# Kernel optimization log

Measured on AMD Instinct MI355X. Metric: run time of the kernel, lower is better.

Reference implementation:

```python
import jax, jax.numpy as jnp
import numpy as np

B, S, D, H, E, K = 2, 2048, 1024, 8, 4, 2
DH = D // H  # 128


def setup_inputs() -> dict:
    key = jax.random.key(0)
    ks = jax.random.split(key, 9)
    std = 1.0 / np.sqrt(D)
    return {
        "q_src": jax.random.normal(ks[0], (B, S, D), jnp.float32),
        "k_src": jax.random.normal(ks[1], (B, S, D), jnp.float32),
        "v_src": jax.random.normal(ks[2], (B, S, D), jnp.float32),
        "Wq": jax.random.normal(ks[3], (H * DH, D), jnp.float32) * std,
        "Wk": jax.random.normal(ks[4], (H * DH, D), jnp.float32) * std,
        "Wv": jax.random.normal(ks[5], (H, E, D, DH), jnp.float32) * std,   # per-head, per-expert V proj
        "Wo": jax.random.normal(ks[6], (H, E, DH, D), jnp.float32) * (1.0 / np.sqrt(H * DH)),
        "sel_v": jax.random.normal(ks[7], (H * E, D), jnp.float32) * std,   # V-expert router
        "sel_o": jax.random.normal(ks[8], (H * E, D), jnp.float32) * std,   # O-expert router
    }


def reference(q_src, k_src, v_src, Wq, Wk, Wv, Wo, sel_v, sel_o):
    s = DH ** -0.25  # scale.sqrt() applied to both q and k -> combined 1/sqrt(d_head)

    q = (q_src @ Wq.T * s).reshape(B, S, H, DH).transpose(0, 2, 1, 3)  # [B,H,S,DH]
    k = (k_src @ Wk.T * s).reshape(B, S, H, DH).transpose(0, 2, 1, 3)

    # --- V expert routing: sigmoid gate + top-k over experts, per head ---
    gv_all = jax.nn.sigmoid((k_src @ sel_v.T).reshape(B, S, H, E))
    gv, iv = jax.lax.top_k(gv_all, K)                                  # [B,S,H,K]
    # per-expert V projection (equiv. to CVMM grouped-GEMM), then gather selected experts
    v_all = jnp.einsum('bsd,hedk->bshek', v_src, Wv)                   # [B,S,H,E,DH]
    v = (jnp.take_along_axis(v_all, iv[..., None], axis=3) * gv[..., None]).sum(3)
    v = v.transpose(0, 2, 1, 3)                                        # [B,H,S,DH]

    # --- attention (mask=None; base class attend() is abstract, plain SDPA) ---
    scores = jnp.einsum('bhqd,bhkd->bhqk', q, k)
    att = jax.nn.softmax(scores, axis=-1)
    res = jnp.einsum('bhqk,bhkd->bhqd', att, v).transpose(0, 2, 1, 3)  # [B,S,H,DH]

    # --- O expert routing: weighted sum over heads and selected output experts ---
    go_all = jax.nn.sigmoid((q_src @ sel_o.T).reshape(B, S, H, E))
    go, io = jax.lax.top_k(go_all, K)                                  # [B,S,H,K]
    gd = (go[..., None] * jax.nn.one_hot(io, E, dtype=res.dtype)).sum(-2)  # dense gates [B,S,H,E]
    gated = res[:, :, :, None, :] * gd[..., None]                      # [B,S,H,E,DH]
    out = jnp.einsum('bshed,hedo->bso', gated, Wo)                     # [B,S,D]
    return out
```

## Files before the change

kernel.cpp:

```cpp
#include <hip/hip_runtime.h>

#define BB 2
#define SS 2048
#define DD 1024
#define HH 8
#define EE 4
#define DHH 128
#define RR (BB*SS)

typedef __attribute__((ext_vector_type(8))) short short8;
typedef __attribute__((ext_vector_type(4))) short short4v;
typedef __attribute__((ext_vector_type(4))) float f32x4;

__device__ __forceinline__ float b2f(short x) {
    unsigned u = ((unsigned)(unsigned short)x) << 16;
    return __uint_as_float(u);
}
__device__ __forceinline__ short f2bf(float f) {
    unsigned u = __float_as_uint(f);
    unsigned r = (u + 0x7fffu + ((u >> 16) & 1u)) >> 16;
    return (short)(unsigned short)r;
}

__device__ __forceinline__ void gl_lds16(const short* g, short* l) {
    __builtin_amdgcn_global_load_lds(
        (const __attribute__((address_space(1))) unsigned int*)g,
        (__attribute__((address_space(3))) unsigned int*)l,
        16, 0, 0);
}

template <bool BF16_OUT>
__device__ __forceinline__ void gemm16_body(
    short* As, short* Bs,
    const short* __restrict__ A, const short* __restrict__ Bm, void* __restrict__ Cv,
    int Kd, int lda, int ldb, int ldc, float alpha, int bm0, int bn0)
{
    const int t = threadIdx.x;
    const int lane = t & 63, wave = t >> 6;
    const int lm = lane & 15, quad = lane >> 4;
    const int wm = (wave >> 1) * 64, wn = (wave & 1) * 64;
    f32x4 acc[4][4] = {};

    const int srow = t >> 2, scol = (t & 3) * 8;
    const short* Ag = A + (long)(bm0 + srow) * lda + scol;
    const short* Bg = Bm + (long)(bn0 + srow) * ldb + scol;
    const long ldaH = (long)lda * 64, ldbH = (long)ldb * 64;
    short* Asd = As + srow * 32 + scol;
    short* Bsd = Bs + srow * 32 + scol;

    for (int k0 = 0; k0 < Kd; k0 += 32) {
        __syncthreads();
        gl_lds16(Ag + k0,        Asd);
        gl_lds16(Ag + k0 + ldaH, Asd + 64 * 32);
        gl_lds16(Bg + k0,        Bsd);
        gl_lds16(Bg + k0 + ldbH, Bsd + 64 * 32);
        __syncthreads();

        short8 af[4], bf[4];
#pragma unroll
        for (int i = 0; i < 4; i++)
            af[i] = *(const short8*)&As[(wm + i * 16 + lm) * 32 + quad * 8];
#pragma unroll
        for (int j = 0; j < 4; j++)
            bf[j] = *(const short8*)&Bs[(wn + j * 16 + lm) * 32 + quad * 8];
#pragma unroll
        for (int i = 0; i < 4; i++)
#pragma unroll
            for (int j = 0; j < 4; j++)
                acc[i][j] = __builtin_amdgcn_mfma_f32_16x16x32_bf16(
                    af[i], bf[j], acc[i][j], 0, 0, 0);
    }
#pragma unroll
    for (int i = 0; i < 4; i++) {
#pragma unroll
        for (int j = 0; j < 4; j++) {
            int n = bn0 + wn + j * 16 + lm;
#pragma unroll
            for (int r = 0; r < 4; r++) {
                int m = bm0 + wm + i * 16 + quad * 4 + r;
                float v = acc[i][j][r] * alpha;
                if (BF16_OUT) ((short*)Cv)[(long)m * ldc + n] = f2bf(v);
                else          ((float*)Cv)[(long)m * ldc + n] = v;
            }
        }
    }
}

__global__ __launch_bounds__(256)
void shc_gemm_bt16(const short* __restrict__ A, const short* __restrict__ Bm,
                   void* __restrict__ Cv, int Kd, int lda, int ldb, int ldc,
                   float alpha)
{
    __shared__ short As[128 * 32];
    __shared__ short Bs[128 * 32];
    gemm16_body<true>(As, Bs, A, Bm, Cv, Kd, lda, ldb, ldc, alpha,
                      blockIdx.y * 128, blockIdx.x * 128);
}

__global__ __launch_bounds__(256)
void shc_gemm_qk(const short* __restrict__ Qs, const short* __restrict__ Ks,
                 const short* __restrict__ Wq16, const short* __restrict__ Wk16,
                 short* __restrict__ Qo, short* __restrict__ Ko, float alpha)
{
    __shared__ short As[128 * 32];
    __shared__ short Bs[128 * 32];
    if (blockIdx.z == 0)
        gemm16_body<true>(As, Bs, Qs, Wq16, Qo, 1024, 1024, 1024, 1024,
                          alpha, blockIdx.y * 128, blockIdx.x * 128);
    else
        gemm16_body<true>(As, Bs, Ks, Wk16, Ko, 1024, 1024, 1024, 1024,
                          alpha, blockIdx.y * 128, blockIdx.x * 128);
}

__global__ __launch_bounds__(256)
void shc_gemm_out(const short* __restrict__ X, const short* __restrict__ WoT,
                  float* __restrict__ out, float* __restrict__ P1)
{
    __shared__ short As[128 * 32];
    __shared__ short Bs[128 * 32];
    const int koff = blockIdx.z * 2048;
    float* C = blockIdx.z ? P1 : out;
    gemm16_body<false>(As, Bs, X + koff, WoT + koff, C,
                       2048, 4096, 4096, 1024, 1.0f,
                       blockIdx.y * 128, blockIdx.x * 128);
}

__global__ __launch_bounds__(256)
void shc_add(float* __restrict__ out, const float* __restrict__ P1)
{
    long i = ((long)blockIdx.x * 256 + threadIdx.x) * 4;
    f32x4 a = *(const f32x4*)(out + i);
    f32x4 b = *(const f32x4*)(P1 + i);
#pragma unroll
    for (int j = 0; j < 4; j++) a[j] += b[j];
    *(f32x4*)(out + i) = a;
}

__global__ __launch_bounds__(256)
void shc_cvt3(const float* __restrict__ a, const float* __restrict__ b,
              const float* __restrict__ c, short* __restrict__ oa,
              short* __restrict__ ob, short* __restrict__ oc)
{
    const float* src = blockIdx.z == 0 ? a : (blockIdx.z == 1 ? b : c);
    short* dst       = blockIdx.z == 0 ? oa : (blockIdx.z == 1 ? ob : oc);
    long i = ((long)blockIdx.x * 256 + threadIdx.x) * 8;
    f32x4 f0 = *(const f32x4*)(src + i);
    f32x4 f1 = *(const f32x4*)(src + i + 4);
    short8 o;
#pragma unroll
    for (int j = 0; j < 4; j++) {
        o[j]     = f2bf(f0[j]);
        o[4 + j] = f2bf(f1[j]);
    }
    *(short8*)(dst + i) = o;
}

__global__ __launch_bounds__(256)
void shc_gates4(const float* __restrict__ q_src, const float* __restrict__ k_src,
                const float* __restrict__ sel_v, const float* __restrict__ sel_o,
                float* __restrict__ gv_d, float* __restrict__ go_d)
{
    const int t = threadIdx.x, lane = t & 63, wave = t >> 6;
    const int bid = blockIdx.x;
    const int s = bid & 1;
    const int r0 = (bid >> 1) * 8 + wave * 2;
    const float* srcb = s ? q_src : k_src;
    const float* selb = s ? sel_o : sel_v;

    double S0[16], S1[16];
#pragma unroll
    for (int i = 0; i < 4; i++) {
        f32x4 v0 = *(const f32x4*)(srcb + (long)r0 * 1024 + lane * 16 + i * 4);
        f32x4 v1 = *(const f32x4*)(srcb + (long)(r0 + 1) * 1024 + lane * 16 + i * 4);
#pragma unroll
        for (int j = 0; j < 4; j++) {
            S0[i * 4 + j] = (double)v0[j];
            S1[i * 4 + j] = (double)v1[j];
        }
    }

    float myv = 0.f;
#pragma unroll 2
    for (int o = 0; o < 32; ++o) {
        f32x4 W[4];
#pragma unroll
        for (int i = 0; i < 4; i++)
            W[i] = *(const f32x4*)(selb + o * 1024 + lane * 16 + i * 4);
        double a0 = 0.0, a1 = 0.0;
#pragma unroll
        for (int i = 0; i < 4; i++)
#pragma unroll
            for (int j = 0; j < 4; j++) {
                double w = (double)W[i][j];
                a0 += S0[i * 4 + j] * w;
                a1 += S1[i * 4 + j] * w;
            }
        a0 += __shfl_xor(a0, 1);  a1 += __shfl_xor(a1, 1);
        a0 += __shfl_xor(a0, 2);  a1 += __shfl_xor(a1, 2);
        a0 += __shfl_xor(a0, 4);  a1 += __shfl_xor(a1, 4);
        a0 += __shfl_xor(a0, 8);  a1 += __shfl_xor(a1, 8);
        a0 += __shfl_xor(a0, 16); a1 += __shfl_xor(a1, 16);
        double tcross = (lane < 32) ? a1 : a0;
        double u = __shfl_xor(tcross, 32);
        double tot = ((lane < 32) ? a0 : a1) + u;
        myv = ((lane & 31) == o) ? (float)tot : myv;
    }

    float sg = 1.f / (1.f + __expf(-myv));
    float g1 = __shfl_xor(sg, 1);
    float g2 = __shfl_xor(sg, 2);
    float g3 = __shfl_xor(sg, 3);
    const int e = lane & 3;
    int rank = 0;
    rank += (g1 > sg) || (g1 == sg && (e ^ 1) < e);
    rank += (g2 > sg) || (g2 == sg && (e ^ 2) < e);
    rank += (g3 > sg) || (g3 == sg && (e ^ 3) < e);
    const long row = r0 + (lane >> 5);
    float* outp = (s ? go_d : gv_d) + row * 32 + (lane & 31);
    *outp = (rank < 2) ? sg : 0.f;
}

__global__ __launch_bounds__(256)
void shc_transpose_w(const float* __restrict__ Wv, short* __restrict__ WvT,
                     const float* __restrict__ Wo, short* __restrict__ WoT)
{
    __shared__ float Ls[32][33];
    const int t = threadIdx.x;
    const int rr = t >> 3, cc = (t & 7) * 4;
    const int bid = blockIdx.x;
    if (bid < 4096) {
        const int dhT = bid & 3, dT = (bid >> 2) & 31, he = bid >> 7;
        const int d0 = dT * 32, dh0 = dhT * 32;
        f32x4 vin = *(const f32x4*)(Wv + (long)(he * 1024 + d0 + rr) * 128 + dh0 + cc);
#pragma unroll
        for (int j = 0; j < 4; j++) Ls[rr][cc + j] = vin[j];
        __syncthreads();
        short4v ov;
#pragma unroll
        for (int j = 0; j < 4; j++) ov[j] = f2bf(Ls[cc + j][rr]);
        *(short4v*)(WvT + (long)(he * 128 + dh0 + rr) * 1024 + d0 + cc) = ov;
    } else {
        const int b2 = bid - 4096;
        const int oT = b2 & 31, kT = b2 >> 5;
        const int k0 = kT * 32, o0 = oT * 32;
        f32x4 vin = *(const f32x4*)(Wo + (long)(k0 + rr) * 1024 + o0 + cc);
#pragma unroll
        for (int j = 0; j < 4; j++) Ls[rr][cc + j] = vin[j];
        __syncthreads();
        short4v ov;
#pragma unroll
        for (int j = 0; j < 4; j++) ov[j] = f2bf(Ls[cc + j][rr]);
        *(short4v*)(WoT + (long)(o0 + rr) * 4096 + k0 + cc) = ov;
    }
}

__global__ __launch_bounds__(256)
void shc_combine_vt(const short* __restrict__ v_all, const float* __restrict__ gv_d,
                    short* __restrict__ Vt)
{
    __shared__ short Ls[64 * 136];
    const int t = threadIdx.x;
    const int blk = blockIdx.x;
    const int st = blk & 31, h = (blk >> 5) & 7, b = blk >> 8;
    const int s0 = st * 64;
    const int sl = t >> 2, dh0 = (t & 3) * 32;
    const long row = (long)(b * SS) + s0 + sl;
    const float* g = gv_d + row * 32 + h * 4;
    float g0 = g[0], g1 = g[1], g2 = g[2], g3 = g[3];
    const short* va = v_all + row * 4096 + h * 512;
#pragma unroll
    for (int j = 0; j < 4; j++) {
        int dh = dh0 + j * 8;
        short8 e0 = *(const short8*)(va + 0 * 128 + dh);
        short8 e1 = *(const short8*)(va + 1 * 128 + dh);
        short8 e2 = *(const short8*)(va + 2 * 128 + dh);
        short8 e3 = *(const short8*)(va + 3 * 128 + dh);
        short8 outv;
#pragma unroll
        for (int i = 0; i < 8; i++)
            outv[i] = f2bf(g0 * b2f(e0[i]) + g1 * b2f(e1[i])
                         + g2 * b2f(e2[i]) + g3 * b2f(e3[i]));
        *(short8*)&Ls[sl * 136 + dh] = outv;
    }
    __syncthreads();
    const int dh = t >> 1, sc0 = (t & 1) * 32;
    short* op = Vt + ((long)(b * HH + h) * DHH + dh) * SS + s0 + sc0;
#pragma unroll
    for (int j = 0; j < 4; j++) {
        short8 ov;
#pragma unroll
        for (int i = 0; i < 8; i++)
            ov[i] = Ls[(sc0 + j * 8 + i) * 136 + dh];
        *(short8*)(op + j * 8) = ov;
    }
}

__global__ __launch_bounds__(256)
void shc_attn_mfma(const short* __restrict__ Q, const short* __restrict__ Kg,
                   const short* __restrict__ Vt, const float* __restrict__ go_d,
                   short* __restrict__ X)
{
    __shared__ __align__(16) char smem[40960];
    short* Ks = (short*)smem;
    short* Vs = (short*)(smem + 16384);
    const int t = threadIdx.x;
    const int lane = t & 63, wave = t >> 6;
    const int lm = lane & 15, quad = lane >> 4;
    short* Pw = (short*)(smem + 32768) + wave * 16 * 64;
    const int blk = blockIdx.x;
    const int qt = blk & 31, h = (blk >> 5) & 7, b = blk >> 8;
    const int q0 = qt * 64 + wave * 16;
    const short* Qb = Q + ((long)(b * SS) + q0) * DD + h * DHH;
    const short* Kb = Kg + (long)(b * SS) * DD + h * DHH;
    const short* Vb = Vt + (long)(b * HH + h) * DHH * SS;

    short8 af[4];
#pragma unroll
    for (int c = 0; c < 4; c++)
        af[c] = *(const short8*)(Qb + (long)lm * DD + c * 32 + quad * 8);

    f32x4 o_acc[8] = {};
    float l_lane[4] = {0.f, 0.f, 0.f, 0.f};

    const int ksrow = t >> 2, kscol = (t & 3) * 32;
    const int vsrow = t >> 1, vscol = (t & 1) * 32;
    const int kswz = (ksrow & 7) << 3;
    const int vswz = (vsrow & 7) << 3;
    const int lmswz = (lm & 7) << 3;

    short8 kv[4], vv[4];
#pragma unroll
    for (int j = 0; j < 4; j++) {
        kv[j] = *(const short8*)(Kb + (long)ksrow * DD + kscol + j * 8);
        vv[j] = *(const short8*)(Vb + (long)vsrow * SS + vscol + j * 8);
    }

    for (int kt = 0; kt < SS / 64; ++kt) {
        __syncthreads();
#pragma unroll
        for (int j = 0; j < 4; j++) {
            *(short8*)&Ks[ksrow * 128 + ((kscol + j * 8) ^ kswz)] = kv[j];
            *(short8*)&Vs[vsrow * 64  + ((vscol + j * 8) ^ vswz)] = vv[j];
        }
        __syncthreads();

        const int ktn = (kt + 1) & 31;
#pragma unroll
        for (int j = 0; j < 4; j++) {
            kv[j] = *(const short8*)(Kb + (long)(ktn * 64 + ksrow) * DD + kscol + j * 8);
            vv[j] = *(const short8*)(Vb + (long)vsrow * SS + ktn * 64 + vscol + j * 8);
        }

#pragma unroll
        for (int f = 0; f < 4; f++) {
            f32x4 acc = {-10.f, -10.f, -10.f, -10.f};
#pragma unroll
            for (int c = 0; c < 4; c++) {
                short8 bf = *(const short8*)&Ks[(f * 16 + lm) * 128
                                                + ((c * 32 + quad * 8) ^ lmswz)];
                acc = __builtin_amdgcn_mfma_f32_16x16x32_bf16(af[c], bf, acc, 0, 0, 0);
            }
#pragma unroll
            for (int r = 0; r < 4; r++) {
                float p = __expf(acc[r]);
                l_lane[r] += p;
                const int prow = quad * 4 + r;
                Pw[prow * 64 + ((f * 16 + lm) ^ ((prow & 7) << 3))] = f2bf(p);
            }
        }

        short8 ap0 = *(const short8*)&Pw[lm * 64 + ((quad * 8) ^ lmswz)];
        short8 ap1 = *(const short8*)&Pw[lm * 64 + ((32 + quad * 8) ^ lmswz)];
#pragma unroll
        for (int d = 0; d < 8; d++) {
            short8 bv0 = *(const short8*)&Vs[(d * 16 + lm) * 64 + ((quad * 8) ^ lmswz)];
            short8 bv1 = *(const short8*)&Vs[(d * 16 + lm) * 64 + ((32 + quad * 8) ^ lmswz)];
            o_acc[d] = __builtin_amdgcn_mfma_f32_16x16x32_bf16(ap0, bv0, o_acc[d], 0, 0, 0);
            o_acc[d] = __builtin_amdgcn_mfma_f32_16x16x32_bf16(ap1, bv1, o_acc[d], 0, 0, 0);
        }
    }

    float inv_r[4];
#pragma unroll
    for (int r = 0; r < 4; r++) {
        float l = l_lane[r];
        l += __shfl_xor(l, 1);
        l += __shfl_xor(l, 2);
        l += __shfl_xor(l, 4);
        l += __shfl_xor(l, 8);
        inv_r[r] = 1.f / l;
    }

    __syncthreads();
    float* Of = (float*)smem;
#pragma unroll
    for (int r = 0; r < 4; r++) {
#pragma unroll
        for (int d = 0; d < 8; d++)
            Of[(wave * 16 + quad * 4 + r) * 132 + d * 16 + lm] = o_acc[d][r] * inv_r[r];
    }
    __syncthreads();
    const int xr = t >> 2, xc0 = (t & 3) * 8;
    const long grow = (long)(b * SS) + qt * 64 + xr;
    const float* go4 = go_d + grow * 32 + h * 4;
    float gg[4] = {go4[0], go4[1], go4[2], go4[3]};
    short* Xp = X + grow * 4096 + h * 512;
#pragma unroll
    for (int e = 0; e < 4; e++) {
#pragma unroll
        for (int j = 0; j < 4; j++) {
            int c = xc0 + 32 * j;
            f32x4 f0 = *(const f32x4*)&Of[xr * 132 + c];
            f32x4 f1 = *(const f32x4*)&Of[xr * 132 + c + 4];
            short8 s;
#pragma unroll
            for (int i = 0; i < 4; i++) {
                s[i]     = f2bf(f0[i] * gg[e]);
                s[4 + i] = f2bf(f1[i] * gg[e]);
            }
            *(short8*)(Xp + e * 128 + c) = s;
        }
    }
}

extern "C" void kernel_launch(void* const* d_in, const int* in_sizes, int n_in,
                              void* d_out, int out_size, void* d_ws, size_t ws_size,
                              hipStream_t stream)
{
    const float* q_src = (const float*)d_in[0];
    const float* k_src = (const float*)d_in[1];
    const float* v_src = (const float*)d_in[2];
    const float* Wq    = (const float*)d_in[3];
    const float* Wk    = (const float*)d_in[4];
    const float* Wv    = (const float*)d_in[5];
    const float* Wo    = (const float*)d_in[6];
    const float* sel_v = (const float*)d_in[7];
    const float* sel_o = (const float*)d_in[8];
    float* out = (float*)d_out;
    char* ws = (char*)d_ws;

    short* Qb16 = (short*)(ws + 0);
    short* Kb16 = (short*)(ws + 8388608);
    short* Vtg  = (short*)(ws + 16777216);
    short* Vs16 = (short*)(ws + 16777216);
    short* Vall = (short*)(ws + 25165824);
    short* X    = (short*)(ws + 25165824);
    short* Wq16 = (short*)(ws + 25165824);
    short* Wk16 = (short*)(ws + 27262976);
    float* P1   = (float*)(ws + 58720256);
    short* Qs16 = (short*)(ws + 58720256);
    short* Ks16 = (short*)(ws + 67108864);
    short* WvT  = (short*)(ws + 75497472);
    short* WoT  = (short*)(ws + 83886080);
    float* GVd  = (float*)(ws + 92274688);
    float* GOd  = (float*)(ws + 92798976);

    const float s_scale = 0.29730177875068026f;

    dim3 blk(256);
    shc_cvt3<<<dim3(2048, 1, 3), blk, 0, stream>>>(q_src, k_src, v_src, Qs16, Ks16, Vs16);
    shc_cvt3<<<dim3(512, 1, 2), blk, 0, stream>>>(Wq, Wk, Wk, Wq16, Wk16, Wk16);
    shc_gemm_qk<<<dim3(8, 32, 2), blk, 0, stream>>>(Qs16, Ks16, Wq16, Wk16, Qb16, Kb16, s_scale);
    shc_gates4<<<1024, blk, 0, stream>>>(q_src, k_src, sel_v, sel_o, GVd, GOd);
    shc_transpose_w<<<8192, blk, 0, stream>>>(Wv, WvT, Wo, WoT);
    shc_gemm_bt16<<<dim3(32, 32), blk, 0, stream>>>(Vs16, WvT, Vall, 1024, 1024, 1024, 4096, 1.0f);
    shc_combine_vt<<<512, blk, 0, stream>>>(Vall, GVd, Vtg);
    shc_attn_mfma<<<512, blk, 0, stream>>>(Qb16, Kb16, Vtg, GOd, X);
    shc_gemm_out<<<dim3(8, 32, 2), blk, 0, stream>>>(X, WoT, out, P1);
    shc_add<<<4096, blk, 0, stream>>>(out, P1);
}
```

Measured before the change: 410.3 us.

## Process 32 query rows per wave, load K/V tiles via direct LDS loads, fold log2e

The attention kernel now handles 128 query rows per block (32 per wave as two 16-row MFMA sub-blocks), so each K/V tile staged in LDS is reused by twice as many queries and the grid is halved to 256 blocks. The register-staged K/V prefetch is replaced by direct global-to-LDS loads (gl_lds16) with XOR swizzled addressing, which drops the software double-buffer. The log2(e) factor is folded into the Q/K scale so the kernel can use exp2f instead of __expf. In exchange there is higher register pressure (launch_bounds 256,1), less latency hiding because global loads are no longer overlapped with compute, and only 256 blocks to spread across the device.

Measured after the change: 426.4 us. +3.9%, slower.

```diff
diff --git a/kernel.cpp b/kernel.cpp
--- a/kernel.cpp
+++ b/kernel.cpp
@@ -295,130 +295,142 @@
     }
 }
 
-__global__ __launch_bounds__(256)
+#define NEG10L2E -14.426950408889634f
+__global__ __launch_bounds__(256, 1)
 void shc_attn_mfma(const short* __restrict__ Q, const short* __restrict__ Kg,
                    const short* __restrict__ Vt, const float* __restrict__ go_d,
                    short* __restrict__ X)
 {
-    __shared__ __align__(16) char smem[40960];
+    __shared__ __align__(16) char smem[49152];
     short* Ks = (short*)smem;
     short* Vs = (short*)(smem + 16384);
     const int t = threadIdx.x;
     const int lane = t & 63, wave = t >> 6;
     const int lm = lane & 15, quad = lane >> 4;
-    short* Pw = (short*)(smem + 32768) + wave * 16 * 64;
+    short* Pw = (short*)(smem + 32768) + wave * 2048;
     const int blk = blockIdx.x;
-    const int qt = blk & 31, h = (blk >> 5) & 7, b = blk >> 8;
-    const int q0 = qt * 64 + wave * 16;
+    const int qt = blk & 15, h = (blk >> 4) & 7, b = blk >> 7;
+    const int q0 = qt * 128 + wave * 32;
     const short* Qb = Q + ((long)(b * SS) + q0) * DD + h * DHH;
     const short* Kb = Kg + (long)(b * SS) * DD + h * DHH;
     const short* Vb = Vt + (long)(b * HH + h) * DHH * SS;
 
-    short8 af[4];
-#pragma unroll
-    for (int c = 0; c < 4; c++)
-        af[c] = *(const short8*)(Qb + (long)lm * DD + c * 32 + quad * 8);
-
-    f32x4 o_acc[8] = {};
-    float l_lane[4] = {0.f, 0.f, 0.f, 0.f};
-
-    const int ksrow = t >> 2, kscol = (t & 3) * 32;
-    const int vsrow = t >> 1, vscol = (t & 1) * 32;
-    const int kswz = (ksrow & 7) << 3;
-    const int vswz = (vsrow & 7) << 3;
+    short8 af[2][4];
+#pragma unroll
+    for (int qb = 0; qb < 2; qb++)
+#pragma unroll
+        for (int c = 0; c < 4; c++)
+            af[qb][c] = *(const short8*)(Qb + (long)(qb * 16 + lm) * DD + c * 32 + quad * 8);
+
+    f32x4 o_acc[2][8] = {};
+    float l_lane[2][4] = {};
+
     const int lmswz = (lm & 7) << 3;
-
-    short8 kv[4], vv[4];
-#pragma unroll
-    for (int j = 0; j < 4; j++) {
-        kv[j] = *(const short8*)(Kb + (long)ksrow * DD + kscol + j * 8);
-        vv[j] = *(const short8*)(Vb + (long)vsrow * SS + vscol + j * 8);
-    }
+    const int w16 = wave * 16, w32 = wave * 32;
+
+    const int rK = lane >> 4;
+    const int colKe = ((lane & 15) * 8) ^ (rK << 3);
+    const int colKo = colKe ^ 32;
+    const int rV = lane >> 3;
+    const int colV = ((lane & 7) * 8) ^ (rV << 3);
 
     for (int kt = 0; kt < SS / 64; ++kt) {
         __syncthreads();
 #pragma unroll
-        for (int j = 0; j < 4; j++) {
-            *(short8*)&Ks[ksrow * 128 + ((kscol + j * 8) ^ kswz)] = kv[j];
-            *(short8*)&Vs[vsrow * 64  + ((vscol + j * 8) ^ vswz)] = vv[j];
-        }
-        __syncthreads();
-
-        const int ktn = (kt + 1) & 31;
-#pragma unroll
-        for (int j = 0; j < 4; j++) {
-            kv[j] = *(const short8*)(Kb + (long)(ktn * 64 + ksrow) * DD + kscol + j * 8);
-            vv[j] = *(const short8*)(Vb + (long)vsrow * SS + ktn * 64 + vscol + j * 8);
-        }
+        for (int i = 0; i < 4; i++) {
+            const short* kg = Kb + (long)(kt * 64 + w16 + i * 4 + rK) * DD
+                              + ((i & 1) ? colKo : colKe);
+            gl_lds16(kg, Ks + (w16 + i * 4) * 128);
+            const short* vg = Vb + (long)(w32 + i * 8 + rV) * SS + kt * 64 + colV;
+            gl_lds16(vg, Vs + (w32 + i * 8) * 64);
+        }
+        __syncthreads();
 
 #pragma unroll
         for (int f = 0; f < 4; f++) {
-            f32x4 acc = {-10.f, -10.f, -10.f, -10.f};
+            f32x4 a0 = {NEG10L2E, NEG10L2E, NEG10L2E, NEG10L2E};
+            f32x4 a1 = a0;
 #pragma unroll
             for (int c = 0; c < 4; c++) {
                 short8 bf = *(const short8*)&Ks[(f * 16 + lm) * 128
                                                 + ((c * 32 + quad * 8) ^ lmswz)];
-                acc = __builtin_amdgcn_mfma_f32_16x16x32_bf16(af[c], bf, acc, 0, 0, 0);
+                a0 = __builtin_amdgcn_mfma_f32_16x16x32_bf16(af[0][c], bf, a0, 0, 0, 0);
+                a1 = __builtin_amdgcn_mfma_f32_16x16x32_bf16(af[1][c], bf, a1, 0, 0, 0);
             }
 #pragma unroll
             for (int r = 0; r < 4; r++) {
-                float p = __expf(acc[r]);
-                l_lane[r] += p;
-                const int prow = quad * 4 + r;
-                Pw[prow * 64 + ((f * 16 + lm) ^ ((prow & 7) << 3))] = f2bf(p);
+                const int pr = quad * 4 + r;
+                const int psw = (pr & 7) << 3;
+                float p0 = exp2f(a0[r]);
+                l_lane[0][r] += p0;
+                Pw[pr * 64 + ((f * 16 + lm) ^ psw)] = f2bf(p0);
+                float p1 = exp2f(a1[r]);
+                l_lane[1][r] += p1;
+                Pw[(16 + pr) * 64 + ((f * 16 + lm) ^ psw)] = f2bf(p1);
             }
         }
 
-        short8 ap0 = *(const short8*)&Pw[lm * 64 + ((quad * 8) ^ lmswz)];
-        short8 ap1 = *(const short8*)&Pw[lm * 64 + ((32 + quad * 8) ^ lmswz)];
+        short8 ap[2][2];
+#pragma unroll
+        for (int qb = 0; qb < 2; qb++) {
+            ap[qb][0] = *(const short8*)&Pw[(qb * 16 + lm) * 64 + ((quad * 8) ^ lmswz)];
+            ap[qb][1] = *(const short8*)&Pw[(qb * 16 + lm) * 64 + ((32 + quad * 8) ^ lmswz)];
+        }
 #pragma unroll
         for (int d = 0; d < 8; d++) {
             short8 bv0 = *(const short8*)&Vs[(d * 16 + lm) * 64 + ((quad * 8) ^ lmswz)];
             short8 bv1 = *(const short8*)&Vs[(d * 16 + lm) * 64 + ((32 + quad * 8) ^ lmswz)];
-            o_acc[d] = __builtin_amdgcn_mfma_f32_16x16x32_bf16(ap0, bv0, o_acc[d], 0, 0, 0);
-            o_acc[d] = __builtin_amdgcn_mfma_f32_16x16x32_bf16(ap1, bv1, o_acc[d], 0, 0, 0);
-        }
-    }
-
-    float inv_r[4];
-#pragma unroll
-    for (int r = 0; r < 4; r++) {
-        float l = l_lane[r];
-        l += __shfl_xor(l, 1);
-        l += __shfl_xor(l, 2);
-        l += __shfl_xor(l, 4);
-        l += __shfl_xor(l, 8);
-        inv_r[r] = 1.f / l;
-    }
-
-    __syncthreads();
+            o_acc[0][d] = __builtin_amdgcn_mfma_f32_16x16x32_bf16(ap[0][0], bv0, o_acc[0][d], 0, 0, 0);
+            o_acc[0][d] = __builtin_amdgcn_mfma_f32_16x16x32_bf16(ap[0][1], bv1, o_acc[0][d], 0, 0, 0);
+            o_acc[1][d] = __builtin_amdgcn_mfma_f32_16x16x32_bf16(ap[1][0], bv0, o_acc[1][d], 0, 0, 0);
+            o_acc[1][d] = __builtin_amdgcn_mfma_f32_16x16x32_bf16(ap[1][1], bv1, o_acc[1][d], 0, 0, 0);
+        }
+    }
+
+    float inv_r[2][4];
+#pragma unroll
+    for (int qb = 0; qb < 2; qb++)
+#pragma unroll
+        for (int r = 0; r < 4; r++) {
+            float l = l_lane[qb][r];
+            l += __shfl_xor(l, 1);
+            l += __shfl_xor(l, 2);
+            l += __shfl_xor(l, 4);
+            l += __shfl_xor(l, 8);
+            inv_r[qb][r] = 1.f / l;
+        }
+
     float* Of = (float*)smem;
 #pragma unroll
-    for (int r = 0; r < 4; r++) {
-#pragma unroll
-        for (int d = 0; d < 8; d++)
-            Of[(wave * 16 + quad * 4 + r) * 132 + d * 16 + lm] = o_acc[d][r] * inv_r[r];
-    }
-    __syncthreads();
-    const int xr = t >> 2, xc0 = (t & 3) * 8;
-    const long grow = (long)(b * SS) + qt * 64 + xr;
-    const float* go4 = go_d + grow * 32 + h * 4;
-    float gg[4] = {go4[0], go4[1], go4[2], go4[3]};
-    short* Xp = X + grow * 4096 + h * 512;
-#pragma unroll
-    for (int e = 0; e < 4; e++) {
-#pragma unroll
-        for (int j = 0; j < 4; j++) {
-            int c = xc0 + 32 * j;
-            f32x4 f0 = *(const f32x4*)&Of[xr * 132 + c];
-            f32x4 f1 = *(const f32x4*)&Of[xr * 132 + c + 4];
-            short8 s;
-#pragma unroll
-            for (int i = 0; i < 4; i++) {
-                s[i]     = f2bf(f0[i] * gg[e]);
-                s[4 + i] = f2bf(f1[i] * gg[e]);
+    for (int hb = 0; hb < 2; hb++) {
+        __syncthreads();
+#pragma unroll
+        for (int r = 0; r < 4; r++) {
+#pragma unroll
+            for (int d = 0; d < 8; d++)
+                Of[(w16 + quad * 4 + r) * 132 + d * 16 + lm] = o_acc[hb][d][r] * inv_r[hb][r];
+        }
+        __syncthreads();
+        const int xr = t >> 2, xc0 = (t & 3) * 8;
+        const long grow = (long)(b * SS) + qt * 128 + (xr >> 4) * 32 + hb * 16 + (xr & 15);
+        const float* go4 = go_d + grow * 32 + h * 4;
+        float gg[4] = {go4[0], go4[1], go4[2], go4[3]};
+        short* Xp = X + grow * 4096 + h * 512;
+#pragma unroll
+        for (int e = 0; e < 4; e++) {
+#pragma unroll
+            for (int j = 0; j < 4; j++) {
+                int c = xc0 + 32 * j;
+                f32x4 f0 = *(const f32x4*)&Of[xr * 132 + c];
+                f32x4 f1 = *(const f32x4*)&Of[xr * 132 + c + 4];
+                short8 s;
+#pragma unroll
+                for (int i = 0; i < 4; i++) {
+                    s[i]     = f2bf(f0[i] * gg[e]);
+                    s[4 + i] = f2bf(f1[i] * gg[e]);
+                }
+                *(short8*)(Xp + e * 128 + c) = s;
             }
-            *(short8*)(Xp + e * 128 + c) = s;
         }
     }
 }
@@ -455,7 +467,7 @@
     float* GVd  = (float*)(ws + 92274688);
     float* GOd  = (float*)(ws + 92798976);
 
-    const float s_scale = 0.29730177875068026f;
+    const float s_scale = 0.29730177875068026f * 1.2011224087864498f;
 
     dim3 blk(256);
     shc_cvt3<<<dim3(2048, 1, 3), blk, 0, stream>>>(q_src, k_src, v_src, Qs16, Ks16, Vs16);
@@ -465,7 +477,7 @@
     shc_transpose_w<<<8192, blk, 0, stream>>>(Wv, WvT, Wo, WoT);
     shc_gemm_bt16<<<dim3(32, 32), blk, 0, stream>>>(Vs16, WvT, Vall, 1024, 1024, 1024, 4096, 1.0f);
     shc_combine_vt<<<512, blk, 0, stream>>>(Vall, GVd, Vtg);
-    shc_attn_mfma<<<512, blk, 0, stream>>>(Qb16, Kb16, Vtg, GOd, X);
+    shc_attn_mfma<<<256, blk, 0, stream>>>(Qb16, Kb16, Vtg, GOd, X);
     shc_gemm_out<<<dim3(8, 32, 2), blk, 0, stream>>>(X, WoT, out, P1);
     shc_add<<<4096, blk, 0, stream>>>(out, P1);
 }
```
